# Kernel tuning notes

Hardware: AMD Instinct MI355X
Metric: run time of the kernel (lower is better)

Reference implementation:

```python
import jax, jax.numpy as jnp
import numpy as np

B, S, DIN, DOUT = 2, 2048, 4096, 4096


def setup_inputs() -> dict:
    key = jax.random.key(0)
    k1, k2, k3, k4, k5 = jax.random.split(key, 5)
    x = jax.random.normal(k1, (B, S, DIN), dtype=jnp.float32)
    # int8-range weights stored as int32 (faithful to q_int_weight.float() upcast)
    q_int_weight = jax.random.randint(k2, (DIN, DOUT), 0, 256, dtype=jnp.int32)
    scale = jax.random.uniform(k3, (1,), dtype=jnp.float32) * 0.01 + 0.001
    zero_point = jax.random.uniform(k4, (1,), dtype=jnp.float32) * 128.0
    bias = jax.random.normal(k5, (DOUT,), dtype=jnp.float32)
    return {"x": x, "q_int_weight": q_int_weight, "scale": scale,
            "zero_point": zero_point, "bias": bias}


def reference(x, q_int_weight, scale, zero_point, bias):
    # Dequantize: (q - zero_point) * scale, per-tensor affine. Stored [in, out].
    w = (q_int_weight.astype(jnp.float32) - zero_point) * scale  # [DIN, DOUT]
    # F.linear(x_flat, w.t(), bias) == x @ w + bias
    y = jnp.einsum('bsi,io->bso', x, w) + bias  # [B, S, DOUT]
    return y
```

## Files before the change

### kernel.cpp

```cpp
#include <hip/hip_runtime.h>
#include <cstdint>
#include <cstddef>

#define M_DIM 4096
#define N_DIM 4096
#define K_DIM 4096
#define BM 256
#define BN 256
#define BKB 128
#define KTILES (K_DIM / BKB)

typedef __attribute__((ext_vector_type(4))) int i32x4;

__device__ __forceinline__ void async_copy16(const void* g, void* l) {
  __builtin_amdgcn_global_load_lds(
      (const __attribute__((address_space(1))) void*)g,
      (__attribute__((address_space(3))) void*)l,
      16, 0, 0);
}

__device__ __forceinline__ void wait_vm6() {
  asm volatile("s_waitcnt vmcnt(6)" ::: "memory");
}
__device__ __forceinline__ void wait_vm4() {
  asm volatile("s_waitcnt vmcnt(4)" ::: "memory");
}
__device__ __forceinline__ void wait_vm2() {
  asm volatile("s_waitcnt vmcnt(2)" ::: "memory");
}
__device__ __forceinline__ void wait_vm0() {
  asm volatile("s_waitcnt vmcnt(0)" ::: "memory");
}
__device__ __forceinline__ void wait_none() {}

__global__ __launch_bounds__(256) void convert_x_kernel(
    const float* __restrict__ x, signed char* __restrict__ xi,
    float* __restrict__ sx, float* __restrict__ rs) {
  __shared__ float red[8];
  const int t = threadIdx.x;
  const size_t row = blockIdx.x;
  const float* xr = x + row * (size_t)K_DIM;

  float4 v[4];
  float amax = 0.f;
#pragma unroll
  for (int i = 0; i < 4; ++i) {
    v[i] = *(const float4*)(xr + (i * 256 + t) * 4);
    amax = fmaxf(amax, fmaxf(fmaxf(fabsf(v[i].x), fabsf(v[i].y)),
                             fmaxf(fabsf(v[i].z), fabsf(v[i].w))));
  }
#pragma unroll
  for (int o = 32; o > 0; o >>= 1)
    amax = fmaxf(amax, __shfl_down(amax, o, 64));
  if ((t & 63) == 0) red[t >> 6] = amax;
  __syncthreads();
  amax = fmaxf(fmaxf(fmaxf(red[0], red[1]), fmaxf(red[2], red[3])), 1e-20f);
  const float inv = 127.f / amax;

  int ssum = 0;
  signed char* out = xi + row * (size_t)K_DIM;
#pragma unroll
  for (int i = 0; i < 4; ++i) {
    const int ia = __float2int_rn(v[i].x * inv);
    const int ib = __float2int_rn(v[i].y * inv);
    const int ic = __float2int_rn(v[i].z * inv);
    const int id = __float2int_rn(v[i].w * inv);
    ssum += ia + ib + ic + id;
    const int pk =
        (ia & 255) | ((ib & 255) << 8) | ((ic & 255) << 16) | (id << 24);
    *(int*)(out + (i * 256 + t) * 4) = pk;
  }
  float fs = (float)ssum;
#pragma unroll
  for (int o = 32; o > 0; o >>= 1) fs += __shfl_down(fs, o, 64);
  if ((t & 63) == 0) red[4 + (t >> 6)] = fs;
  __syncthreads();
  if (t == 0) {
    rs[row] = red[4] + red[5] + red[6] + red[7];
    sx[row] = amax * (1.f / 127.f);
  }
}

__global__ __launch_bounds__(256) void convert_w_kernel(
    const int* __restrict__ q, signed char* __restrict__ qsT) {
  __shared__ __align__(16) int qtile[64][68];
  const int t = threadIdx.x;
  const int k0 = (blockIdx.x & 63) << 6;
  const int n0 = (blockIdx.x >> 6) << 6;

  {
    const int c = t & 15;
    const int r0 = t >> 4;
#pragma unroll
    for (int i = 0; i < 4; ++i) {
      const int r = r0 + i * 16;
      const int4 v = *(const int4*)(q + (size_t)(k0 + r) * N_DIM + n0 + c * 4);
      *(int4*)&qtile[r][c * 4] = v;
    }
  }
  __syncthreads();
  {
    const int kc = t & 15;
    const int g = t >> 4;
    int4 v[4];
#pragma unroll
    for (int i = 0; i < 4; ++i) v[i] = *(const int4*)&qtile[kc * 4 + i][g * 4];
#pragma unroll
    for (int j = 0; j < 4; ++j) {
      const int b0 = ((&v[0].x)[j] - 128) & 255;
      const int b1 = ((&v[1].x)[j] - 128) & 255;
      const int b2 = ((&v[2].x)[j] - 128) & 255;
      const int b3 = ((&v[3].x)[j] - 128) & 255;
      const int pk = b0 | (b1 << 8) | (b2 << 16) | (b3 << 24);
      *(int*)(qsT + (size_t)(n0 + g * 4 + j) * K_DIM + k0 + kc * 4) = pk;
    }
  }
}

__global__ __launch_bounds__(512, 2) void gemm_kernel(
    const signed char* __restrict__ A,
    const signed char* __restrict__ Bt,
    const float* __restrict__ bias, const float* __restrict__ sx,
    const float* __restrict__ rs, const float* __restrict__ scale_p,
    const float* __restrict__ zp_p, float* __restrict__ C) {
  __shared__ __align__(16) signed char As[2][BM * BKB];
  __shared__ __align__(16) signed char Bs[2][BN * BKB];

  const int tid = threadIdx.x;
  const int wave = tid >> 6;
  const int lane = tid & 63;
  const int wm = wave >> 2;
  const int wn = wave & 3;

  const int swz = (blockIdx.x & 7) * 32 + (blockIdx.x >> 3);
  const int bm = swz & 15;
  const int bn = swz >> 4;
  const size_t m0 = (size_t)bm * BM;
  const size_t n0 = (size_t)bn * BN;

  const int srow = lane >> 3;
  const int schunk = (lane & 7) ^ srow;

  const int quad = lane >> 4;
  const int lrow = lane & 15;
  const int rsw = lrow & 7;

  const signed char* Abase = A + m0 * K_DIM + schunk * 16;
  const signed char* Bbase = Bt + n0 * K_DIM + schunk * 16;

  i32x4 acc[8][4];
  const i32x4 zero = {0, 0, 0, 0};
#pragma unroll
  for (int i = 0; i < 8; ++i)
#pragma unroll
    for (int j = 0; j < 4; ++j) acc[i][j] = zero;

  auto stageA = [&](int b, int k0, int ig) {
#pragma unroll
    for (int i = 0; i < 2; ++i) {
      const int rbase = i * 128 + ig * 64 + wave * 8;
      const size_t go = (size_t)(rbase + srow) * K_DIM + k0;
      async_copy16(Abase + go, (void*)&As[b][rbase * BKB]);
    }
  };
  auto stageB = [&](int b, int k0, int jg) {
#pragma unroll
    for (int i = 0; i < 2; ++i) {
      const int rbase = (i * 2 + (wave >> 2)) * 64 + jg * 32 + (wave & 3) * 8;
      const size_t go = (size_t)(rbase + srow) * K_DIM + k0;
      async_copy16(Bbase + go, (void*)&Bs[b][rbase * BKB]);
    }
  };

#define LDA(ig)                                                              \
  do {                                                                       \
    _Pragma("unroll") for (int kh = 0; kh < 2; ++kh)                         \
        _Pragma("unroll") for (int t = 0; t < 4; ++t) {                      \
      const int ar = wm * 128 + (ig) * 64 + t * 16 + lrow;                   \
      av[kh][t] =                                                            \
          *(const i32x4*)(as + ar * BKB + ((((kh << 2) | quad) ^ rsw) << 4));\
    }                                                                        \
  } while (0)

#define LDB(jg)                                                              \
  do {                                                                       \
    _Pragma("unroll") for (int kh = 0; kh < 2; ++kh)                         \
        _Pragma("unroll") for (int t = 0; t < 2; ++t) {                      \
      const int br = wn * 64 + ((jg) * 2 + t) * 16 + lrow;                   \
      bv[kh][(jg) * 2 + t] =                                                 \
          *(const i32x4*)(bs + br * BKB + ((((kh << 2) | quad) ^ rsw) << 4));\
    }                                                                        \
  } while (0)

#define MFMA16(ibase, j0)                                                    \
  do {                                                                       \
    __builtin_amdgcn_s_setprio(1);                                           \
    _Pragma("unroll") for (int kh = 0; kh < 2; ++kh)                         \
        _Pragma("unroll") for (int t = 0; t < 4; ++t)                        \
            _Pragma("unroll") for (int j = 0; j < 2; ++j)                    \
        acc[(ibase) + t][(j0) + j] = __builtin_amdgcn_mfma_i32_16x16x64_i8(  \
            av[kh][t], bv[kh][(j0) + j], acc[(ibase) + t][(j0) + j], 0, 0,   \
            0);                                                              \
    __builtin_amdgcn_s_setprio(0);                                           \
  } while (0)

#define DO_TILE(AS, BS, S0, W0, S1, W1, S2, W2, S3)                          \
  do {                                                                       \
    const signed char* as = (AS);                                            \
    const signed char* bs = (BS);                                            \
    i32x4 av[2][4], bv[2][4];                                                \
    LDA(0);                                                                  \
    LDB(0);                                                                  \
    S0;                                                                      \
    W0();                                                                    \
    __builtin_amdgcn_s_barrier();                                            \
    MFMA16(0, 0);                                                            \
    __builtin_amdgcn_s_barrier();                                            \
    LDB(1);                                                                  \
    S1;                                                                      \
    W1();                                                                    \
    __builtin_amdgcn_s_barrier();                                            \
    MFMA16(0, 2);                                                            \
    __builtin_amdgcn_s_barrier();                                            \
    LDA(1);                                                                  \
    S2;                                                                      \
    W2();                                                                    \
    __builtin_amdgcn_s_barrier();                                            \
    MFMA16(4, 2);                                                            \
    __builtin_amdgcn_s_barrier();                                            \
    S3;                                                                      \
    MFMA16(4, 0);                                                            \
  } while (0)

  stageA(0, 0, 0);
  stageB(0, 0, 0);
  stageB(0, 0, 1);
  stageA(0, 0, 1);
  stageA(1, BKB, 0);
  stageB(1, BKB, 0);
  stageB(1, BKB, 1);
  wait_vm6();
  __builtin_amdgcn_s_barrier();

#pragma unroll 2
  for (int kt = 0; kt < KTILES - 2; ++kt) {
    const int buf = kt & 1;
    const int k1 = (kt + 1) * BKB;
    const int k2 = (kt + 2) * BKB;
    DO_TILE(As[buf], Bs[buf],
            (stageA(buf ^ 1, k1, 1)), wait_vm6,
            (stageA(buf, k2, 0)),     wait_vm6,
            (stageB(buf, k2, 0)),     wait_vm6,
            (stageB(buf, k2, 1)));
  }

  DO_TILE(As[0], Bs[0], (stageA(1, 31 * BKB, 1)), wait_vm6, (void)0, wait_vm4,
          (void)0, wait_vm2, (void)0);
  DO_TILE(As[1], Bs[1], (void)0, wait_vm0, (void)0, wait_none, (void)0,
          wait_none, (void)0);

#undef LDA
#undef LDB
#undef MFMA16
#undef DO_TILE

  const float scale = scale_p[0];
  const float c1 = 128.f - zp_p[0];
#pragma unroll
  for (int i = 0; i < 8; ++i) {
    const size_t mbase = m0 + wm * 128 + i * 16 + quad * 4;
    float am[4], bmv[4];
#pragma unroll
    for (int r = 0; r < 4; ++r) {
      const float a = scale * sx[mbase + r];
      am[r] = a;
      bmv[r] = a * c1 * rs[mbase + r];
    }
#pragma unroll
    for (int j = 0; j < 4; ++j) {
      const size_t n = n0 + wn * 64 + j * 16 + lrow;
      const float bv = bias[n];
#pragma unroll
      for (int r = 0; r < 4; ++r) {
        C[(mbase + r) * N_DIM + n] =
            fmaf(am[r], (float)acc[i][j][r], bmv[r] + bv);
      }
    }
  }
}

extern "C" void kernel_launch(void* const* d_in, const int* in_sizes, int n_in,
                              void* d_out, int out_size, void* d_ws,
                              size_t ws_size, hipStream_t stream) {
  const float* x = (const float*)d_in[0];
  const int* q = (const int*)d_in[1];
  const float* scale = (const float*)d_in[2];
  const float* zp = (const float*)d_in[3];
  const float* bias = (const float*)d_in[4];
  float* out = (float*)d_out;

  char* ws = (char*)d_ws;
  signed char* xi = (signed char*)ws;
  signed char* qsT = (signed char*)(ws + ((size_t)16 << 20));
  float* sx = (float*)(ws + ((size_t)32 << 20));
  float* rs = (float*)(ws + ((size_t)32 << 20) + (16 << 10));

  convert_x_kernel<<<4096, 256, 0, stream>>>(x, xi, sx, rs);
  convert_w_kernel<<<4096, 256, 0, stream>>>(q, qsT);
  gemm_kernel<<<256, 512, 0, stream>>>(xi, qsT, bias, sx, rs, scale, zp, out);
}
```

Baseline: 252.4 us.

## Collapse per-phase vmcnt waits into one wait and barrier per K tile

Replaces the three staggered s_waitcnt/barrier pairs inside each K-tile with a single vmcnt wait and barrier at the top of the tile. The prologue wait and the tail-specific vm4/vm2 waits are removed to match. LDS fragment loads (LDB(1), LDA(1)) are hoisted so they overlap the MFMA groups, and each tile has fewer barriers. The aim is less barrier and wait stalling between MFMA groups. The cost is higher register pressure from keeping more fragments live, and correctness depends on the remaining barriers still ordering the staged writes against the shared-memory reads.

```diff
diff --git a/kernel.cpp b/kernel.cpp
--- a/kernel.cpp
+++ b/kernel.cpp
@@ -22,16 +22,9 @@
 __device__ __forceinline__ void wait_vm6() {
   asm volatile("s_waitcnt vmcnt(6)" ::: "memory");
 }
-__device__ __forceinline__ void wait_vm4() {
-  asm volatile("s_waitcnt vmcnt(4)" ::: "memory");
-}
-__device__ __forceinline__ void wait_vm2() {
-  asm volatile("s_waitcnt vmcnt(2)" ::: "memory");
-}
 __device__ __forceinline__ void wait_vm0() {
   asm volatile("s_waitcnt vmcnt(0)" ::: "memory");
 }
-__device__ __forceinline__ void wait_none() {}
 
 __global__ __launch_bounds__(256) void convert_x_kernel(
     const float* __restrict__ x, signed char* __restrict__ xi,
@@ -199,37 +192,34 @@
         _Pragma("unroll") for (int t = 0; t < 4; ++t)                        \
             _Pragma("unroll") for (int j = 0; j < 2; ++j)                    \
         acc[(ibase) + t][(j0) + j] = __builtin_amdgcn_mfma_i32_16x16x64_i8(  \
-            av[kh][t], bv[kh][(j0) + j], acc[(ibase) + t][(j0) + j], 0, 0,   \
-            0);                                                              \
+            af_mfma(t, kh), bv[kh][(j0) + j], acc[(ibase) + t][(j0) + j], 0, \
+            0, 0);                                                           \
     __builtin_amdgcn_s_setprio(0);                                           \
   } while (0)
-
-#define DO_TILE(AS, BS, S0, W0, S1, W1, S2, W2, S3)                          \
+#define af_mfma(t, kh) av[kh][t]
+
+#define DO_TILE(AS, BS, TOPW, S0, S1, S2, S3)                                \
   do {                                                                       \
     const signed char* as = (AS);                                            \
     const signed char* bs = (BS);                                            \
     i32x4 av[2][4], bv[2][4];                                                \
+    TOPW();                                                                  \
+    __builtin_amdgcn_s_barrier();                                            \
     LDA(0);                                                                  \
     LDB(0);                                                                  \
+    LDB(1);                                                                  \
     S0;                                                                      \
-    W0();                                                                    \
-    __builtin_amdgcn_s_barrier();                                            \
-    MFMA16(0, 0);                                                            \
-    __builtin_amdgcn_s_barrier();                                            \
-    LDB(1);                                                                  \
+    MFMA16(0, 0);                                         \
+    __builtin_amdgcn_s_barrier();                                            \
     S1;                                                                      \
-    W1();                                                                    \
-    __builtin_amdgcn_s_barrier();                                            \
-    MFMA16(0, 2);                                                            \
-    __builtin_amdgcn_s_barrier();                                            \
-    LDA(1);                                                                  \
+    MFMA16(0, 2);                                         \
+    LDA(1);         \
+    __builtin_amdgcn_s_barrier();                                            \
     S2;                                                                      \
-    W2();                                                                    \
-    __builtin_amdgcn_s_barrier();                                            \
-    MFMA16(4, 2);                                                            \
+    MFMA16(4, 2);                                         \
     __builtin_amdgcn_s_barrier();                                            \
     S3;                                                                      \
-    MFMA16(4, 0);                                                            \
+    MFMA16(4, 0);                                         \
   } while (0)
 
   stageA(0, 0, 0);
@@ -239,29 +229,27 @@
   stageA(1, BKB, 0);
   stageB(1, BKB, 0);
   stageB(1, BKB, 1);
-  wait_vm6();
-  __builtin_amdgcn_s_barrier();
 
 #pragma unroll 2
   for (int kt = 0; kt < KTILES - 2; ++kt) {
     const int buf = kt & 1;
     const int k1 = (kt + 1) * BKB;
     const int k2 = (kt + 2) * BKB;
-    DO_TILE(As[buf], Bs[buf],
-            (stageA(buf ^ 1, k1, 1)), wait_vm6,
-            (stageA(buf, k2, 0)),     wait_vm6,
-            (stageB(buf, k2, 0)),     wait_vm6,
+    DO_TILE(As[buf], Bs[buf], wait_vm6,
+            (stageA(buf ^ 1, k1, 1)),
+            (stageA(buf, k2, 0)),
+            (stageB(buf, k2, 0)),
             (stageB(buf, k2, 1)));
   }
 
-  DO_TILE(As[0], Bs[0], (stageA(1, 31 * BKB, 1)), wait_vm6, (void)0, wait_vm4,
-          (void)0, wait_vm2, (void)0);
-  DO_TILE(As[1], Bs[1], (void)0, wait_vm0, (void)0, wait_none, (void)0,
-          wait_none, (void)0);
+  DO_TILE(As[0], Bs[0], wait_vm6, (stageA(1, 31 * BKB, 1)), (void)0, (void)0,
+          (void)0);
+  DO_TILE(As[1], Bs[1], wait_vm0, (void)0, (void)0, (void)0, (void)0);
 
 #undef LDA
 #undef LDB
 #undef MFMA16
+#undef af_mfma
 #undef DO_TILE
 
   const float scale = scale_p[0];
```

New measurement: 241.9 us. 4.2% less time.
